# Performance work log

Hardware: AMD Instinct MI355X
Metric: run time of the kernel (lower is better)

Reference implementation:

```python
import jax, jax.numpy as jnp
import numpy as np

N = 20000      # nodes
E = 640000     # edges
FIN = 256
FQK = 256


def setup_inputs() -> dict:
    key = jax.random.key(0)
    kx, ks, kd, kw = jax.random.split(key, 4)
    x = jax.random.normal(kx, (N, FIN), dtype=jnp.float32)
    # src must be sorted (original scatter_softmax assumes grouped index);
    # force last element to N-1 so nbatches == N as in batch[-1]+1.
    src = jnp.sort(jax.random.randint(ks, (E,), 0, N))
    src = src.at[-1].set(N - 1)
    dest = jax.random.randint(kd, (E,), 0, N)
    ei = jnp.stack([src, dest]).astype(jnp.int64)
    # nn.Linear(Fin, 2*Fqk, bias=False) weight: [2*Fqk, Fin]
    bound = 1.0 / np.sqrt(FIN)
    W = jax.random.uniform(kw, (2 * FQK, FIN), dtype=jnp.float32,
                           minval=-bound, maxval=bound)
    return {"x": x, "ei": ei, "W": W}


def reference(x, ei, W):
    src, dest = ei[0], ei[1]
    n_nodes = x.shape[0]
    scaling = FQK ** -0.5
    qk = x @ W.T                      # [N, 2*Fqk]
    q, k = jnp.split(qk, 2, axis=-1)  # each [N, Fqk]
    q = q * scaling
    # per-edge dot product: (q[src] . k[dest])  -> [E]
    aw = jnp.einsum('ef,ef->e', q[src], k[dest])
    # scatter softmax over edges grouped by src node (raw exp, as original)
    ex = jnp.exp(aw)
    expsum = jax.ops.segment_sum(ex, src, num_segments=n_nodes)  # [N]
    return ex / expsum[src]
```

## Files before the change

### kernel.cpp

```cpp
#include <hip/hip_runtime.h>
#include <cmath>

#define FIN 256
#define FQK 256
#define SCALING 0.0625f
#define MAX_SEG 256

typedef __bf16 bf16_t;
typedef bf16_t bf16x8 __attribute__((ext_vector_type(8)));
typedef float  f32x4  __attribute__((ext_vector_type(4)));

__device__ __forceinline__ unsigned short f2bf(float f) {
    unsigned int u = __float_as_uint(f);
    u += 0x7FFFu + ((u >> 16) & 1u);
    return (unsigned short)(u >> 16);
}
__device__ __forceinline__ float bf_lo(unsigned int w) { return __uint_as_float(w << 16); }
__device__ __forceinline__ float bf_hi(unsigned int w) { return __uint_as_float(w & 0xFFFF0000u); }

__global__ __launch_bounds__(FIN) void compute_M_kernel(const float* __restrict__ W,
                                                        unsigned short* __restrict__ Mb) {
    const int f = blockIdx.x;
    const int g = threadIdx.x;
    const float* __restrict__ Wq = W;
    const float* __restrict__ Wk = W + FQK * FIN;
    float acc = 0.f;
#pragma unroll 8
    for (int c = 0; c < FQK; ++c) {
        acc += Wq[c * FIN + f] * Wk[c * FIN + g];
    }
    Mb[f * FIN + g] = f2bf(acc * SCALING);
}

#define ASTRIDE 40

__global__ __launch_bounds__(256) void gemm_y_kernel(const float* __restrict__ x,
                                                     const unsigned short* __restrict__ Mb,
                                                     unsigned short* __restrict__ y, int N) {
    __shared__ unsigned short sA[64 * ASTRIDE];

    const int t    = threadIdx.x;
    const int wv   = t >> 6;
    const int lane = t & 63;
    const int q    = lane >> 4;
    const int m16  = lane & 15;
    const int n0   = blockIdx.x * 64;
    const int f0   = wv * 64;

    f32x4 acc[4][4] = {};

    const int srow = t >> 2;
    const int skc  = (t & 3) * 8;

    for (int kc = 0; kc < FIN; kc += 32) {
        {
            const int n = n0 + srow;
            float4 v0 = make_float4(0.f, 0.f, 0.f, 0.f), v1 = v0;
            if (n < N) {
                v0 = *(const float4*)(x + (size_t)n * FIN + kc + skc);
                v1 = *(const float4*)(x + (size_t)n * FIN + kc + skc + 4);
            }
            unsigned short* p = &sA[srow * ASTRIDE + skc];
            p[0] = f2bf(v0.x); p[1] = f2bf(v0.y); p[2] = f2bf(v0.z); p[3] = f2bf(v0.w);
            p[4] = f2bf(v1.x); p[5] = f2bf(v1.y); p[6] = f2bf(v1.z); p[7] = f2bf(v1.w);
        }
        __syncthreads();

        bf16x8 afrag[4];
#pragma unroll
        for (int mt = 0; mt < 4; ++mt) {
            const int row = mt * 16 + m16;
            afrag[mt] = *(const bf16x8*)&sA[row * ASTRIDE + q * 8];
        }
#pragma unroll
        for (int ft = 0; ft < 4; ++ft) {
            const int f = f0 + ft * 16 + m16;
            union { uint4 u; bf16x8 v; } bu;
            bu.u = *(const uint4*)(Mb + (size_t)f * FIN + kc + q * 8);
#pragma unroll
            for (int mt = 0; mt < 4; ++mt)
                acc[mt][ft] = __builtin_amdgcn_mfma_f32_16x16x32_bf16(afrag[mt], bu.v,
                                                                     acc[mt][ft], 0, 0, 0);
        }
        __syncthreads();
    }

#pragma unroll
    for (int mt = 0; mt < 4; ++mt) {
#pragma unroll
        for (int r = 0; r < 4; ++r) {
            const int n = n0 + mt * 16 + q * 4 + r;
            if (n < N) {
#pragma unroll
                for (int ft = 0; ft < 4; ++ft)
                    y[(size_t)n * FIN + f0 + ft * 16 + m16] = f2bf(acc[mt][ft][r]);
            }
        }
    }
}

__global__ __launch_bounds__(256) void seg_kernel(const int* __restrict__ src,
                                                  int* __restrict__ seg, int N, int E) {
    const int n = blockIdx.x * 256 + threadIdx.x;
    if (n > N) return;
    int lo = 0, hi = E;
    while (lo < hi) {
        const int mid = (lo + hi) >> 1;
        if (src[mid] < n) lo = mid + 1; else hi = mid;
    }
    seg[n] = lo;
}

__global__ __launch_bounds__(256) void node_edge_kernel(const float* __restrict__ x,
                                                        const unsigned short* __restrict__ y,
                                                        const int* __restrict__ dest,
                                                        const int* __restrict__ seg,
                                                        float* __restrict__ out, int N) {
    __shared__ float exlds[4][MAX_SEG];

    const int w    = threadIdx.x >> 6;
    const int lane = threadIdx.x & 63;
    const int n    = blockIdx.x * 4 + w;
    const int g    = lane >> 4;
    const int j    = lane & 15;

    int   s0 = 0, cnt = 0;
    float inv = 0.f;

    if (n < N) {
        s0 = seg[n];
        cnt = seg[n + 1] - s0;
    }

    if (cnt > 0) {
        float4 xf[4];
#pragma unroll
        for (int u = 0; u < 2; ++u) {
            xf[u * 2 + 0] = *(const float4*)(x + (size_t)n * FIN + u * 128 + j * 8);
            xf[u * 2 + 1] = *(const float4*)(x + (size_t)n * FIN + u * 128 + j * 8 + 4);
        }

        float sum = 0.f;
        for (int base = 0; base < cnt; base += 64) {
            const int m = min(64, cnt - base);
            const int vd = (lane < m) ? dest[s0 + base + lane] : 0;
            const int nit = (m + 3) >> 2;
            for (int it = 0; it < nit; ++it) {
                const int  eg    = it * 4 + g;
                const bool valid = eg < m;
                const int  d     = __shfl(vd, eg, 64);
                const uint4* __restrict__ yr = (const uint4*)(y + (size_t)(valid ? d : 0) * FIN);
                float acc = 0.f;
#pragma unroll
                for (int u = 0; u < 2; ++u) {
                    const uint4 qv = yr[u * 16 + j];
                    const float4 xa = xf[u * 2 + 0];
                    const float4 xb = xf[u * 2 + 1];
                    acc += bf_lo(qv.x) * xa.x + bf_hi(qv.x) * xa.y
                         + bf_lo(qv.y) * xa.z + bf_hi(qv.y) * xa.w
                         + bf_lo(qv.z) * xb.x + bf_hi(qv.z) * xb.y
                         + bf_lo(qv.w) * xb.z + bf_hi(qv.w) * xb.w;
                }
                acc += __shfl_xor(acc, 1, 64);
                acc += __shfl_xor(acc, 2, 64);
                acc += __shfl_xor(acc, 4, 64);
                acc += __shfl_xor(acc, 8, 64);
                if (valid) {
                    const float ex = __expf(acc);
                    sum += ex;
                    const int idx = base + eg;
                    if (j == 0 && idx < MAX_SEG) exlds[w][idx] = ex;
                }
            }
        }
        sum += __shfl_xor(sum, 16, 64);
        sum += __shfl_xor(sum, 32, 64);
        inv = 1.0f / sum;
    }

    __syncthreads();

    if (cnt > 0) {
        const int lim = cnt < MAX_SEG ? cnt : MAX_SEG;
        for (int i = lane; i < lim; i += 64)
            out[s0 + i] = exlds[w][i] * inv;
    }
}

extern "C" void kernel_launch(void* const* d_in, const int* in_sizes, int n_in,
                              void* d_out, int out_size, void* d_ws, size_t ws_size,
                              hipStream_t stream) {
    const float* x  = (const float*)d_in[0];
    const int*   ei = (const int*)d_in[1];
    const float* W  = (const float*)d_in[2];
    float* out = (float*)d_out;

    const int N = in_sizes[0] / FIN;
    const int E = in_sizes[1] / 2;

    unsigned short* Mb = (unsigned short*)d_ws;
    unsigned short* y  = Mb + (size_t)FIN * FIN;
    int*            seg = (int*)(y + (size_t)N * FIN);

    compute_M_kernel<<<FIN, FIN, 0, stream>>>(W, Mb);

    gemm_y_kernel<<<(N + 63) / 64, 256, 0, stream>>>(x, Mb, y, N);

    seg_kernel<<<(N + 256) / 256, 256, 0, stream>>>(ei, seg, N, E);

    node_edge_kernel<<<(N + 3) / 4, 256, 0, stream>>>(x, y, ei + E, seg, out, N);
}
```

Before: 140.0 us.

## Merge M and segment kernels, shrink GEMM tile, widen per-edge gather

The weight-product kernel and the segment binary-search kernel are merged into one launch, which removes a launch and lets the two run concurrently. The y GEMM drops its shared-memory staging and barriers. Each block now covers 16 rows, and every wave loads x directly into registers, converts it to bf16 and issues MFMAs. The node-edge kernel has 8 lanes per edge instead of 16, so each lane holds 32 x values, reads dest directly without the shuffle broadcast, and processes 8 edges per iteration. The cost is less reuse of M loads across rows in the GEMM and more registers per lane.

```diff
diff --git a/kernel.cpp b/kernel.cpp
--- a/kernel.cpp
+++ b/kernel.cpp
@@ -18,97 +18,87 @@
 __device__ __forceinline__ float bf_lo(unsigned int w) { return __uint_as_float(w << 16); }
 __device__ __forceinline__ float bf_hi(unsigned int w) { return __uint_as_float(w & 0xFFFF0000u); }
 
-__global__ __launch_bounds__(FIN) void compute_M_kernel(const float* __restrict__ W,
-                                                        unsigned short* __restrict__ Mb) {
-    const int f = blockIdx.x;
-    const int g = threadIdx.x;
-    const float* __restrict__ Wq = W;
-    const float* __restrict__ Wk = W + FQK * FIN;
-    float acc = 0.f;
-#pragma unroll 8
-    for (int c = 0; c < FQK; ++c) {
-        acc += Wq[c * FIN + f] * Wk[c * FIN + g];
-    }
-    Mb[f * FIN + g] = f2bf(acc * SCALING);
+__device__ __forceinline__ bf16x8 cvt8(float4 a, float4 b) {
+    bf16x8 r;
+    r[0] = (bf16_t)a.x; r[1] = (bf16_t)a.y; r[2] = (bf16_t)a.z; r[3] = (bf16_t)a.w;
+    r[4] = (bf16_t)b.x; r[5] = (bf16_t)b.y; r[6] = (bf16_t)b.z; r[7] = (bf16_t)b.w;
+    return r;
 }
 
-#define ASTRIDE 40
+__global__ __launch_bounds__(256) void m_seg_kernel(const float* __restrict__ W,
+                                                    unsigned short* __restrict__ Mb,
+                                                    const int* __restrict__ src,
+                                                    int* __restrict__ seg, int N, int E) {
+    const int b = blockIdx.x;
+    if (b < FIN) {
+        const int f = b;
+        const int g = threadIdx.x;
+        const float* __restrict__ Wq = W;
+        const float* __restrict__ Wk = W + FQK * FIN;
+        float acc = 0.f;
+#pragma unroll 8
+        for (int c = 0; c < FQK; ++c)
+            acc += Wq[c * FIN + f] * Wk[c * FIN + g];
+        Mb[f * FIN + g] = f2bf(acc * SCALING);
+    } else {
+        const int n = (b - FIN) * 256 + threadIdx.x;
+        if (n > N) return;
+        int lo = 0, hi = E;
+        while (lo < hi) {
+            const int mid = (lo + hi) >> 1;
+            if (src[mid] < n) lo = mid + 1; else hi = mid;
+        }
+        seg[n] = lo;
+    }
+}
 
 __global__ __launch_bounds__(256) void gemm_y_kernel(const float* __restrict__ x,
                                                      const unsigned short* __restrict__ Mb,
                                                      unsigned short* __restrict__ y, int N) {
-    __shared__ unsigned short sA[64 * ASTRIDE];
-
     const int t    = threadIdx.x;
     const int wv   = t >> 6;
     const int lane = t & 63;
     const int q    = lane >> 4;
     const int m16  = lane & 15;
-    const int n0   = blockIdx.x * 64;
+    const int n0   = blockIdx.x * 16;
     const int f0   = wv * 64;
 
-    f32x4 acc[4][4] = {};
+    const int row  = n0 + m16;
+    const int rowc = row < N ? row : N - 1;
+    const float* __restrict__ xr = x + (size_t)rowc * FIN;
 
-    const int srow = t >> 2;
-    const int skc  = (t & 3) * 8;
+    f32x4 acc[4] = {};
 
+#pragma unroll
     for (int kc = 0; kc < FIN; kc += 32) {
-        {
-            const int n = n0 + srow;
-            float4 v0 = make_float4(0.f, 0.f, 0.f, 0.f), v1 = v0;
-            if (n < N) {
-                v0 = *(const float4*)(x + (size_t)n * FIN + kc + skc);
-                v1 = *(const float4*)(x + (size_t)n * FIN + kc + skc + 4);
-            }
-            unsigned short* p = &sA[srow * ASTRIDE + skc];
-            p[0] = f2bf(v0.x); p[1] = f2bf(v0.y); p[2] = f2bf(v0.z); p[3] = f2bf(v0.w);
-            p[4] = f2bf(v1.x); p[5] = f2bf(v1.y); p[6] = f2bf(v1.z); p[7] = f2bf(v1.w);
-        }
-        __syncthreads();
-
-        bf16x8 afrag[4];
-#pragma unroll
-        for (int mt = 0; mt < 4; ++mt) {
-            const int row = mt * 16 + m16;
-            afrag[mt] = *(const bf16x8*)&sA[row * ASTRIDE + q * 8];
-        }
+        const float4 a0 = *(const float4*)(xr + kc + q * 8);
+        const float4 a1 = *(const float4*)(xr + kc + q * 8 + 4);
+        const bf16x8 af = cvt8(a0, a1);
 #pragma unroll
         for (int ft = 0; ft < 4; ++ft) {
             const int f = f0 + ft * 16 + m16;
             union { uint4 u; bf16x8 v; } bu;
             bu.u = *(const uint4*)(Mb + (size_t)f * FIN + kc + q * 8);
-#pragma unroll
-            for (int mt = 0; mt < 4; ++mt)
-                acc[mt][ft] = __builtin_amdgcn_mfma_f32_16x16x32_bf16(afrag[mt], bu.v,
-                                                                     acc[mt][ft], 0, 0, 0);
+            acc[ft] = __builtin_amdgcn_mfma_f32_16x16x32_bf16(af, bu.v, acc[ft], 0, 0, 0);
         }
-        __syncthreads();
     }
 
 #pragma unroll
-    for (int mt = 0; mt < 4; ++mt) {
+    for (int r = 0; r < 4; ++r) {
+        const int n = n0 + q * 4 + r;
+        if (n < N) {
 #pragma unroll
-        for (int r = 0; r < 4; ++r) {
-            const int n = n0 + mt * 16 + q * 4 + r;
-            if (n < N) {
-#pragma unroll
-                for (int ft = 0; ft < 4; ++ft)
-                    y[(size_t)n * FIN + f0 + ft * 16 + m16] = f2bf(acc[mt][ft][r]);
-            }
+            for (int ft = 0; ft < 4; ++ft)
+                y[(size_t)n * FIN + f0 + ft * 16 + m16] = f2bf(acc[ft][r]);
         }
     }
 }
 
-__global__ __launch_bounds__(256) void seg_kernel(const int* __restrict__ src,
-                                                  int* __restrict__ seg, int N, int E) {
-    const int n = blockIdx.x * 256 + threadIdx.x;
-    if (n > N) return;
-    int lo = 0, hi = E;
-    while (lo < hi) {
-        const int mid = (lo + hi) >> 1;
-        if (src[mid] < n) lo = mid + 1; else hi = mid;
-    }
-    seg[n] = lo;
+__device__ __forceinline__ float dot8(uint4 qv, float4 xa, float4 xb) {
+    return bf_lo(qv.x) * xa.x + bf_hi(qv.x) * xa.y
+         + bf_lo(qv.y) * xa.z + bf_hi(qv.y) * xa.w
+         + bf_lo(qv.z) * xb.x + bf_hi(qv.z) * xb.y
+         + bf_lo(qv.w) * xb.z + bf_hi(qv.w) * xb.w;
 }
 
 __global__ __launch_bounds__(256) void node_edge_kernel(const float* __restrict__ x,
@@ -121,58 +111,46 @@
     const int w    = threadIdx.x >> 6;
     const int lane = threadIdx.x & 63;
     const int n    = blockIdx.x * 4 + w;
-    const int g    = lane >> 4;
-    const int j    = lane & 15;
+    const int g    = lane >> 3;
+    const int j    = lane & 7;
 
     int   s0 = 0, cnt = 0;
     float inv = 0.f;
 
     if (n < N) {
-        s0 = seg[n];
+        s0  = seg[n];
         cnt = seg[n + 1] - s0;
     }
 
     if (cnt > 0) {
-        float4 xf[4];
+        float4 xf[8];
+        const float* __restrict__ xr = x + (size_t)n * FIN + j * 32;
 #pragma unroll
-        for (int u = 0; u < 2; ++u) {
-            xf[u * 2 + 0] = *(const float4*)(x + (size_t)n * FIN + u * 128 + j * 8);
-            xf[u * 2 + 1] = *(const float4*)(x + (size_t)n * FIN + u * 128 + j * 8 + 4);
-        }
+        for (int u = 0; u < 8; ++u) xf[u] = *(const float4*)(xr + u * 4);
 
         float sum = 0.f;
-        for (int base = 0; base < cnt; base += 64) {
-            const int m = min(64, cnt - base);
-            const int vd = (lane < m) ? dest[s0 + base + lane] : 0;
-            const int nit = (m + 3) >> 2;
-            for (int it = 0; it < nit; ++it) {
-                const int  eg    = it * 4 + g;
-                const bool valid = eg < m;
-                const int  d     = __shfl(vd, eg, 64);
-                const uint4* __restrict__ yr = (const uint4*)(y + (size_t)(valid ? d : 0) * FIN);
-                float acc = 0.f;
-#pragma unroll
-                for (int u = 0; u < 2; ++u) {
-                    const uint4 qv = yr[u * 16 + j];
-                    const float4 xa = xf[u * 2 + 0];
-                    const float4 xb = xf[u * 2 + 1];
-                    acc += bf_lo(qv.x) * xa.x + bf_hi(qv.x) * xa.y
-                         + bf_lo(qv.y) * xa.z + bf_hi(qv.y) * xa.w
-                         + bf_lo(qv.z) * xb.x + bf_hi(qv.z) * xb.y
-                         + bf_lo(qv.w) * xb.z + bf_hi(qv.w) * xb.w;
-                }
+        const int nit = (cnt + 7) >> 3;
+        for (int it = 0; it < nit; ++it) {
+            const int i = it * 8 + g;
+            if (i < cnt) {
+                const int d = dest[s0 + i];
+                const uint4* __restrict__ yr =
+                    (const uint4*)(y + (size_t)d * FIN) + j * 4;
+                const uint4 q0 = yr[0];
+                const uint4 q1 = yr[1];
+                const uint4 q2 = yr[2];
+                const uint4 q3 = yr[3];
+                float acc = dot8(q0, xf[0], xf[1]) + dot8(q1, xf[2], xf[3])
+                          + dot8(q2, xf[4], xf[5]) + dot8(q3, xf[6], xf[7]);
                 acc += __shfl_xor(acc, 1, 64);
                 acc += __shfl_xor(acc, 2, 64);
                 acc += __shfl_xor(acc, 4, 64);
-                acc += __shfl_xor(acc, 8, 64);
-                if (valid) {
-                    const float ex = __expf(acc);
-                    sum += ex;
-                    const int idx = base + eg;
-                    if (j == 0 && idx < MAX_SEG) exlds[w][idx] = ex;
-                }
+                const float ex = __expf(acc);
+                sum += ex;
+                if (j == 0 && i < MAX_SEG) exlds[w][i] = ex;
             }
         }
+        sum += __shfl_xor(sum, 8, 64);
         sum += __shfl_xor(sum, 16, 64);
         sum += __shfl_xor(sum, 32, 64);
         inv = 1.0f / sum;
@@ -198,15 +176,14 @@
     const int N = in_sizes[0] / FIN;
     const int E = in_sizes[1] / 2;
 
-    unsigned short* Mb = (unsigned short*)d_ws;
-    unsigned short* y  = Mb + (size_t)FIN * FIN;
+    unsigned short* Mb  = (unsigned short*)d_ws;
+    unsigned short* y   = Mb + (size_t)FIN * FIN;
     int*            seg = (int*)(y + (size_t)N * FIN);
 
-    compute_M_kernel<<<FIN, FIN, 0, stream>>>(W, Mb);
+    const int segBlocks = (N + 256) / 256;
+    m_seg_kernel<<<FIN + segBlocks, 256, 0, stream>>>(W, Mb, ei, seg, N, E);
 
-    gemm_y_kernel<<<(N + 63) / 64, 256, 0, stream>>>(x, Mb, y, N);
-
-    seg_kernel<<<(N + 256) / 256, 256, 0, stream>>>(ei, seg, N, E);
+    gemm_y_kernel<<<(N + 15) / 16, 256, 0, stream>>>(x, Mb, y, N);
 
     node_edge_kernel<<<(N + 3) / 4, 256, 0, stream>>>(x, y, ei + E, seg, out, N);
 }
```

Result: slower. 160.9 us (+14.9%).
